# Kernel optimization log

Hardware: AMD Instinct MI355X
Metric: run time of the kernel (lower is better)

The kernel has to match this reference:

```python
import jax, jax.numpy as jnp
import numpy as np

T, G, K, N = 131072, 64, 1024, 512  # batch_sum, batch_count, k, n
M_MAX = 4096  # static upper bound on any group size (setup guarantees <= 3072)
PAD = 128     # tile alignment for padded offsets


def setup_inputs() -> dict:
    key = jax.random.key(0)
    k1, k2 = jax.random.split(key)
    a = jax.random.normal(k1, (T, K), dtype=jnp.float32)
    b = jax.random.normal(k2, (G, K, N), dtype=jnp.float32) / np.float32(np.sqrt(K))
    rng = np.random.default_rng(0)
    d = rng.integers(-1024, 1024, G // 2)
    deltas = np.concatenate([d, -d])
    rng.shuffle(deltas)
    sizes = (T // G) + deltas  # each in [1024, 3072], sums exactly to T
    offsets = np.concatenate([[0], np.cumsum(sizes)[:-1]])
    padded = ((sizes + PAD - 1) // PAD) * PAD
    padded_offsets = np.concatenate([[0], np.cumsum(padded)[:-1]])
    return {
        "a": a,
        "b": b,
        "batch_sizes": jnp.asarray(sizes, dtype=jnp.int32),
        "batch_offsets": jnp.asarray(offsets, dtype=jnp.int32),
        "batch_padded_offsets": jnp.asarray(padded_offsets, dtype=jnp.int32),
    }


def reference(a, b, batch_sizes, batch_offsets, batch_padded_offsets):
    # Grouped GEMM: for each group g, out[off_g : off_g+size_g] = a[rows] @ b[g].
    # jit-friendly: scan over groups with a fixed M_MAX window, mask invalid rows.
    T_, _ = a.shape
    n_out = b.shape[-1]
    iota = jnp.arange(M_MAX)

    def body(out, xs):
        off, size, bg = xs
        rows = jnp.clip(off + iota, 0, T_ - 1)          # [M_MAX]
        mask = iota < size                               # [M_MAX]
        a_g = jnp.where(mask[:, None], a[rows], 0.0)     # [M_MAX, K]
        y = a_g @ bg                                     # [M_MAX, N]
        out = out.at[rows].add(y)                        # masked rows add zeros
        return out, None

    out0 = jnp.zeros((T_, n_out), dtype=a.dtype)
    out, _ = jax.lax.scan(body, out0, (batch_offsets, batch_sizes, b))
    return out
```

## Files before the change

### kernel.cpp

```cpp
#include <hip/hip_runtime.h>
#include <hip/hip_bf16.h>
#include <stdint.h>

#define T_ROWS 131072
#define GCNT   64
#define KDIM   1024
#define NDIM   512
#define BM     128
#define BN     128
#define BK     64
#define KTILES (KDIM / BK)
#define MT_MAX 1088
#define NBLK   (MT_MAX * 4)

typedef __attribute__((ext_vector_type(4))) float f32x4;
typedef __attribute__((ext_vector_type(8))) short s16x8;
typedef __attribute__((ext_vector_type(4))) short s16x4;
typedef __attribute__((address_space(3))) unsigned int lds_u32;
typedef const __attribute__((address_space(1))) unsigned int gbl_u32;

static __device__ __forceinline__ short f2bf(float f) {
  __hip_bfloat16 h = __float2bfloat16(f);
  return __builtin_bit_cast(short, h);
}

__global__ __launch_bounds__(256) void bt_kernel(const float* __restrict__ b,
                                                 char* __restrict__ bt) {
  __shared__ short lt[64 * 130];
  int bid = blockIdx.x;
  int kt = bid & 15, nt = (bid >> 4) & 3, g = bid >> 6;
  int t = threadIdx.x;
  const float* src = b + ((size_t)(g * KDIM + kt * BK)) * NDIM + nt * 128;
#pragma unroll
  for (int i = 0; i < 32; i++) {
    int idx = i * 256 + t;
    int kk = idx >> 7, nn = idx & 127;
    lt[kk * 130 + nn] = f2bf(src[(size_t)kk * NDIM + nn]);
  }
  __syncthreads();
  char* dst = bt + ((size_t)bid << 14);
#pragma unroll
  for (int j = 0; j < 4; j++) {
    int chunk = j * 256 + t;
    int n = chunk >> 3;
    int slot = (chunk & 7) ^ (n & 7);
    s16x8 v;
#pragma unroll
    for (int i = 0; i < 8; i++) v[i] = lt[(slot * 8 + i) * 130 + n];
    *(s16x8*)(dst + (size_t)chunk * 16) = v;
  }
}

__global__ __launch_bounds__(256, 3) void gemm3(
    const float* __restrict__ a, const char* __restrict__ bt,
    const int* __restrict__ sizes, const int* __restrict__ offs,
    float* __restrict__ out) {
  __shared__ __align__(16) short lds_a[BM * BK];
  __shared__ __align__(16) char lds_b[2][BN * BK * 2];

  int bid0 = blockIdx.x;
  int bid = (bid0 & 7) * (NBLK / 8) + (bid0 >> 3);
  int bn = bid & 3;
  int tm = bid >> 2;

  int g = -1, m_loc = 0, base = 0;
#pragma unroll
  for (int i = 0; i < GCNT; i++) {
    int tg = ((sizes[i] + 127) & ~127) >> 7;
    if (tm >= base && tm < base + tg) { g = i; m_loc = (tm - base) << 7; }
    base += tg;
  }
  if (g < 0) return;
  int size = sizes[g], off = offs[g], valid = size - m_loc;

  int t = threadIdx.x, lane = t & 63, wid = t >> 6;
  int wm = wid >> 1, wn = wid & 1, lr = lane & 15, q = lane >> 4;

  int r0 = t >> 4, c16 = t & 15;
  int aoff[8];
#pragma unroll
  for (int i = 0; i < 8; i++) {
    int row = off + m_loc + i * 16 + r0;
    if (row >= T_ROWS) row = T_ROWS - 1;
    aoff[i] = row * KDIM + c16 * 4;
  }
  int a_wbyte = r0 * 128 + (((c16 >> 1) ^ (r0 & 7)) << 4) + (c16 & 1) * 8;

  const char* btimg = bt + ((size_t)((g << 6) + (bn << 4)) << 14);

  f32x4 acc[4][4];
#pragma unroll
  for (int i = 0; i < 4; i++)
#pragma unroll
    for (int j = 0; j < 4; j++) acc[i][j] = (f32x4){0.f, 0.f, 0.f, 0.f};
  f32x4 va[8];

  auto loadA = [&](int kt) {
#pragma unroll
    for (int i = 0; i < 8; i++)
      va[i] = *(const f32x4*)(a + aoff[i] + kt * BK);
  };
  auto writeA = [&]() {
    char* db = (char*)lds_a + a_wbyte;
#pragma unroll
    for (int i = 0; i < 8; i++) {
      s16x4 v;
#pragma unroll
      for (int e = 0; e < 4; e++) v[e] = f2bf(va[i][e]);
      *(s16x4*)(db + i * 2048) = v;
    }
  };
  auto stageB = [&](int kt, int c) {
#pragma unroll
    for (int i = 0; i < 4; i++) {
      int wc = wid * 4 + i;
      int cc = wc * 64 + lane;
      const char* gsrc = btimg + ((size_t)kt << 14) + (size_t)cc * 16;
      __builtin_amdgcn_global_load_lds(
          (gbl_u32*)gsrc, (lds_u32*)((char*)lds_b[c] + wc * 1024), 16, 0, 0);
    }
  };
  auto compute = [&](int c) {
#pragma unroll
    for (int ks = 0; ks < 2; ks++) {
      s16x8 af[4], bf[4];
#pragma unroll
      for (int fm = 0; fm < 4; fm++) {
        int row = wm * 64 + fm * 16 + lr;
        int slot = (ks * 4 + q) ^ (row & 7);
        af[fm] = *(const s16x8*)((const char*)lds_a + row * 128 + slot * 16);
      }
#pragma unroll
      for (int fn = 0; fn < 4; fn++) {
        int n = wn * 64 + fn * 16 + lr;
        int slot = (ks * 4 + q) ^ (n & 7);
        bf[fn] = *(const s16x8*)((const char*)lds_b[c] + n * 128 + slot * 16);
      }
      __builtin_amdgcn_s_setprio(1);
#pragma unroll
      for (int fm = 0; fm < 4; fm++)
#pragma unroll
        for (int fn = 0; fn < 4; fn++)
          acc[fm][fn] = __builtin_amdgcn_mfma_f32_16x16x32_bf16(
              af[fm], bf[fn], acc[fm][fn], 0, 0, 0);
      __builtin_amdgcn_s_setprio(0);
    }
  };

  stageB(0, 0);
  __builtin_amdgcn_sched_barrier(0);
  loadA(0);

  for (int kt = 0; kt < KTILES - 1; kt++) {
    int cur = kt & 1, nxt = cur ^ 1;
    stageB(kt + 1, nxt);
    __builtin_amdgcn_sched_barrier(0);
    writeA();
    loadA(kt + 1);
    asm volatile("s_waitcnt lgkmcnt(0)" ::: "memory");
    __builtin_amdgcn_sched_barrier(0);
    __builtin_amdgcn_s_barrier();
    compute(cur);
    __builtin_amdgcn_sched_barrier(0);
    __builtin_amdgcn_s_barrier();
  }
  writeA();
  asm volatile("s_waitcnt lgkmcnt(0)" ::: "memory");
  __builtin_amdgcn_sched_barrier(0);
  __builtin_amdgcn_s_barrier();
  compute(1);

  size_t orow0 = (size_t)(off + m_loc);
#pragma unroll
  for (int fm = 0; fm < 4; fm++) {
#pragma unroll
    for (int j = 0; j < 4; j++) {
      int rm = wm * 64 + fm * 16 + q * 4 + j;
      if (rm < valid) {
        float* orow = out + (orow0 + rm) * NDIM + bn * BN + wn * 64 + lr;
#pragma unroll
        for (int fn = 0; fn < 4; fn++) orow[fn * 16] = acc[fm][fn][j];
      }
    }
  }
}

__global__ __launch_bounds__(256, 2) void gemm_fb(
    const float* __restrict__ a, const float* __restrict__ b,
    const int* __restrict__ sizes, const int* __restrict__ offs,
    float* __restrict__ out) {
  __shared__ __align__(16) short lds_a2[2][BM * BK];
  __shared__ __align__(16) char lds_b2[2][BN * BK * 2];

  int bid0 = blockIdx.x;
  int bid = (bid0 & 7) * (NBLK / 8) + (bid0 >> 3);
  int bn = bid & 3;
  int tm = bid >> 2;

  int g = -1, m_loc = 0, base = 0;
#pragma unroll
  for (int i = 0; i < GCNT; i++) {
    int tg = ((sizes[i] + 127) & ~127) >> 7;
    if (tm >= base && tm < base + tg) { g = i; m_loc = (tm - base) << 7; }
    base += tg;
  }
  if (g < 0) return;
  int size = sizes[g], off = offs[g], valid = size - m_loc;

  int t = threadIdx.x, lane = t & 63, wid = t >> 6;
  int wm = wid >> 1, wn = wid & 1, lr = lane & 15, q = lane >> 4;

  int r0 = t >> 4, c16 = t & 15;
  int aoff[8];
#pragma unroll
  for (int i = 0; i < 8; i++) {
    int row = off + m_loc + i * 16 + r0;
    if (row >= T_ROWS) row = T_ROWS - 1;
    aoff[i] = row * KDIM + c16 * 4;
  }
  int a_wbyte = r0 * 128 + (((c16 >> 1) ^ (r0 & 7)) << 4) + (c16 & 1) * 8;
  int fb_n = t >> 1, fb_kh = (t & 1) * 32;

  f32x4 acc[4][4];
#pragma unroll
  for (int i = 0; i < 4; i++)
#pragma unroll
    for (int j = 0; j < 4; j++) acc[i][j] = (f32x4){0.f, 0.f, 0.f, 0.f};
  f32x4 va[8];

  auto loadA = [&](int kt) {
#pragma unroll
    for (int i = 0; i < 8; i++) va[i] = *(const f32x4*)(a + aoff[i] + kt * BK);
  };
  auto writeA = [&](int c) {
    char* db = (char*)lds_a2[c] + a_wbyte;
#pragma unroll
    for (int i = 0; i < 8; i++) {
      s16x4 v;
#pragma unroll
      for (int e = 0; e < 4; e++) v[e] = f2bf(va[i][e]);
      *(s16x4*)(db + i * 2048) = v;
    }
  };
  auto stageB = [&](int kt, int c) {
    const float* p = b + (size_t)g * KDIM * NDIM +
                     (size_t)(kt * BK + fb_kh) * NDIM + bn * BN + fb_n;
    float vals[32];
#pragma unroll
    for (int i = 0; i < 32; i++) vals[i] = p[(size_t)i * NDIM];
    char* lb = (char*)lds_b2[c] + fb_n * 128;
#pragma unroll
    for (int i8 = 0; i8 < 4; i8++) {
      int slot = (fb_kh >> 3) + i8;
      s16x8 v;
#pragma unroll
      for (int e = 0; e < 8; e++) v[e] = f2bf(vals[i8 * 8 + e]);
      *(s16x8*)(lb + ((slot ^ (fb_n & 7)) << 4)) = v;
    }
  };
  auto compute = [&](int c) {
#pragma unroll
    for (int ks = 0; ks < 2; ks++) {
      s16x8 af[4], bf[4];
#pragma unroll
      for (int fm = 0; fm < 4; fm++) {
        int row = wm * 64 + fm * 16 + lr;
        int slot = (ks * 4 + q) ^ (row & 7);
        af[fm] = *(const s16x8*)((const char*)lds_a2[c] + row * 128 + slot * 16);
      }
#pragma unroll
      for (int fn = 0; fn < 4; fn++) {
        int n = wn * 64 + fn * 16 + lr;
        int slot = (ks * 4 + q) ^ (n & 7);
        bf[fn] = *(const s16x8*)((const char*)lds_b2[c] + n * 128 + slot * 16);
      }
#pragma unroll
      for (int fm = 0; fm < 4; fm++)
#pragma unroll
        for (int fn = 0; fn < 4; fn++)
          acc[fm][fn] = __builtin_amdgcn_mfma_f32_16x16x32_bf16(
              af[fm], bf[fn], acc[fm][fn], 0, 0, 0);
    }
  };

  loadA(0);
  stageB(0, 0);
  writeA(0);
  __syncthreads();
  for (int kt = 0; kt < KTILES; kt++) {
    int cur = kt & 1, nxt = cur ^ 1;
    bool more = (kt + 1 < KTILES);
    if (more) loadA(kt + 1);
    compute(cur);
    if (more) {
      stageB(kt + 1, nxt);
      writeA(nxt);
      __syncthreads();
    }
  }
  size_t orow0 = (size_t)(off + m_loc);
#pragma unroll
  for (int fm = 0; fm < 4; fm++) {
#pragma unroll
    for (int j = 0; j < 4; j++) {
      int rm = wm * 64 + fm * 16 + q * 4 + j;
      if (rm < valid) {
        float* orow = out + (orow0 + rm) * NDIM + bn * BN + wn * 64 + lr;
#pragma unroll
        for (int fn = 0; fn < 4; fn++) orow[fn * 16] = acc[fm][fn][j];
      }
    }
  }
}

extern "C" void kernel_launch(void* const* d_in, const int* in_sizes, int n_in,
                              void* d_out, int out_size, void* d_ws,
                              size_t ws_size, hipStream_t stream) {
  const float* a = (const float*)d_in[0];
  const float* b = (const float*)d_in[1];
  const int* sizes = (const int*)d_in[2];
  const int* offs = (const int*)d_in[3];
  float* out = (float*)d_out;

  const size_t bt_bytes = (size_t)GCNT * KDIM * NDIM * 2;
  if (ws_size >= bt_bytes) {
    bt_kernel<<<GCNT * 64, 256, 0, stream>>>(b, (char*)d_ws);
    gemm3<<<NBLK, 256, 0, stream>>>(a, (const char*)d_ws, sizes, offs, out);
  } else {
    gemm_fb<<<NBLK, 256, 0, stream>>>(a, b, sizes, offs, out);
  }
}
```

Baseline: 290.0 us.

## Single-buffer B tile in LDS to raise occupancy to four blocks per CU

Replaces the double-buffered B LDS tile with a single buffer, loading B for the current k-tile at the start of each iteration and waiting with a partial vmcnt so only the B loads must land. This cuts LDS use per block so launch bounds can request four blocks per CU instead of three. The trade is that B load latency is no longer prefetched a tile ahead, and the tighter register budget may force spills.

```diff
diff --git a/kernel.cpp b/kernel.cpp
--- a/kernel.cpp
+++ b/kernel.cpp
@@ -51,12 +51,12 @@
   }
 }
 
-__global__ __launch_bounds__(256, 3) void gemm3(
+__global__ __launch_bounds__(256, 4) void gemm9(
     const float* __restrict__ a, const char* __restrict__ bt,
     const int* __restrict__ sizes, const int* __restrict__ offs,
     float* __restrict__ out) {
   __shared__ __align__(16) short lds_a[BM * BK];
-  __shared__ __align__(16) char lds_b[2][BN * BK * 2];
+  __shared__ __align__(16) char lds_b[BN * BK * 2];
 
   int bid0 = blockIdx.x;
   int bid = (bid0 & 7) * (NBLK / 8) + (bid0 >> 3);
@@ -110,17 +110,17 @@
       *(s16x4*)(db + i * 2048) = v;
     }
   };
-  auto stageB = [&](int kt, int c) {
+  auto stageB = [&](int kt) {
 #pragma unroll
     for (int i = 0; i < 4; i++) {
       int wc = wid * 4 + i;
       int cc = wc * 64 + lane;
       const char* gsrc = btimg + ((size_t)kt << 14) + (size_t)cc * 16;
       __builtin_amdgcn_global_load_lds(
-          (gbl_u32*)gsrc, (lds_u32*)((char*)lds_b[c] + wc * 1024), 16, 0, 0);
-    }
-  };
-  auto compute = [&](int c) {
+          (gbl_u32*)gsrc, (lds_u32*)(lds_b + wc * 1024), 16, 0, 0);
+    }
+  };
+  auto compute = [&]() {
 #pragma unroll
     for (int ks = 0; ks < 2; ks++) {
       s16x8 af[4], bf[4];
@@ -134,7 +134,7 @@
       for (int fn = 0; fn < 4; fn++) {
         int n = wn * 64 + fn * 16 + lr;
         int slot = (ks * 4 + q) ^ (n & 7);
-        bf[fn] = *(const s16x8*)((const char*)lds_b[c] + n * 128 + slot * 16);
+        bf[fn] = *(const s16x8*)((const char*)lds_b + n * 128 + slot * 16);
       }
       __builtin_amdgcn_s_setprio(1);
 #pragma unroll
@@ -147,28 +147,28 @@
     }
   };
 
-  stageB(0, 0);
-  __builtin_amdgcn_sched_barrier(0);
   loadA(0);
 
   for (int kt = 0; kt < KTILES - 1; kt++) {
-    int cur = kt & 1, nxt = cur ^ 1;
-    stageB(kt + 1, nxt);
+    stageB(kt);
     __builtin_amdgcn_sched_barrier(0);
     writeA();
     loadA(kt + 1);
+    asm volatile("s_waitcnt vmcnt(8)" ::: "memory");
     asm volatile("s_waitcnt lgkmcnt(0)" ::: "memory");
     __builtin_amdgcn_sched_barrier(0);
     __builtin_amdgcn_s_barrier();
-    compute(cur);
+    compute();
     __builtin_amdgcn_sched_barrier(0);
     __builtin_amdgcn_s_barrier();
   }
+  stageB(15);
+  __builtin_amdgcn_sched_barrier(0);
   writeA();
-  asm volatile("s_waitcnt lgkmcnt(0)" ::: "memory");
+  asm volatile("s_waitcnt vmcnt(0) lgkmcnt(0)" ::: "memory");
   __builtin_amdgcn_sched_barrier(0);
   __builtin_amdgcn_s_barrier();
-  compute(1);
+  compute();
 
   size_t orow0 = (size_t)(off + m_loc);
 #pragma unroll
@@ -230,7 +230,8 @@
 
   auto loadA = [&](int kt) {
 #pragma unroll
-    for (int i = 0; i < 8; i++) va[i] = *(const f32x4*)(a + aoff[i] + kt * BK);
+    for (int i = 0; i < 8; i++)
+      va[i] = *(const f32x4*)(a + aoff[i] + kt * BK);
   };
   auto writeA = [&](int c) {
     char* db = (char*)lds_a2[c] + a_wbyte;
@@ -266,7 +267,8 @@
       for (int fm = 0; fm < 4; fm++) {
         int row = wm * 64 + fm * 16 + lr;
         int slot = (ks * 4 + q) ^ (row & 7);
-        af[fm] = *(const s16x8*)((const char*)lds_a2[c] + row * 128 + slot * 16);
+        af[fm] =
+            *(const s16x8*)((const char*)lds_a2[c] + row * 128 + slot * 16);
       }
 #pragma unroll
       for (int fn = 0; fn < 4; fn++) {
@@ -325,7 +327,7 @@
   const size_t bt_bytes = (size_t)GCNT * KDIM * NDIM * 2;
   if (ws_size >= bt_bytes) {
     bt_kernel<<<GCNT * 64, 256, 0, stream>>>(b, (char*)d_ws);
-    gemm3<<<NBLK, 256, 0, stream>>>(a, (const char*)d_ws, sizes, offs, out);
+    gemm9<<<NBLK, 256, 0, stream>>>(a, (const char*)d_ws, sizes, offs, out);
   } else {
     gemm_fb<<<NBLK, 256, 0, stream>>>(a, b, sizes, offs, out);
   }
```

Measured after the change: 833.3 us. +187.4%, slower.
